# Kernel optimization log

Hardware: AMD Instinct MI355X
Metric: run time of the kernel (lower is better)

The kernel has to match this reference:

```python
import jax, jax.numpy as jnp
import numpy as np
import math

HID = 4096
SLOTS = 8
HEADS = 8
BD = 512  # bottleneck_dim
HD = BD // HEADS  # effective head dim = 64
B, S = 4, 4096


def setup_inputs() -> dict:
    key = jax.random.key(0)
    ks = jax.random.split(key, 8)
    std = 1.0 / math.sqrt(HID)
    return {
        "hidden_states": jax.random.normal(ks[0], (B, S, HID), dtype=jnp.float32),
        "attention_mask": jax.random.randint(ks[1], (B, S), 0, 2, dtype=jnp.int32),
        "memory_slots": jax.random.normal(ks[2], (SLOTS, HID), dtype=jnp.float32) * std,
        # torch nn.Linear weights are [out_features, in_features]
        "Wq": jax.random.normal(ks[3], (BD, HID), dtype=jnp.float32) * std,
        "Wk": jax.random.normal(ks[4], (BD, HID), dtype=jnp.float32) * std,
        "Wv": jax.random.normal(ks[5], (BD, HID), dtype=jnp.float32) * std,
        "Wo": jax.random.normal(ks[6], (HID, BD), dtype=jnp.float32) * (1.0 / math.sqrt(BD)),
    }


def reference(hidden_states, attention_mask, memory_slots, Wq, Wk, Wv, Wo):
    # Q from learnable slots (same for every batch element): [slots, BD]
    Q = memory_slots @ Wq.T
    Q = Q.reshape(SLOTS, HEADS, HD)                      # n h d
    # K/V from sequence: [b, s, BD] -> [b, s, h, d]
    K = jnp.einsum('bsi,oi->bso', hidden_states, Wk).reshape(B, S, HEADS, HD)
    V = jnp.einsum('bsi,oi->bso', hidden_states, Wv).reshape(B, S, HEADS, HD)
    # scores: [b, h, n, s]
    scores = jnp.einsum('nhd,bshd->bhns', Q, K) / jnp.sqrt(jnp.array(HD, scores_dtype := jnp.float32))
    mask = attention_mask[:, None, None, :]              # [b,1,1,s]
    scores = jnp.where(mask == 0, jnp.finfo(scores.dtype).min, scores)
    attn = jax.nn.softmax(scores, axis=-1)
    # output: [b, n, h, d] -> [b, n, BD]
    out = jnp.einsum('bhns,bshd->bnhd', attn, V).reshape(B, SLOTS, BD)
    # o_proj back to hidden_size
    return jnp.einsum('bnd,od->bno', out, Wo)            # [b, slots, HID]
```

## Files before the change

kernel.cpp:

```cpp
#include <hip/hip_runtime.h>
#include <math.h>

#define HID   4096
#define SLOTS 8
#define HEADS 8
#define BD    512
#define HD    64
#define BB    4
#define SS    4096
#define R64   64
#define LSTR  72

typedef __attribute__((ext_vector_type(8))) short bf16x8;
typedef __attribute__((ext_vector_type(4))) float f32x4;

__device__ __forceinline__ unsigned short f2bf(float x) {
  unsigned int u = __builtin_bit_cast(unsigned int, x);
  return (unsigned short)((u + 0x7fffu + ((u >> 16) & 1u)) >> 16);
}

__global__ void q_kernel(const float* __restrict__ ms, const float* __restrict__ Wq,
                         float* __restrict__ Q) {
  int w = (blockIdx.x * blockDim.x + threadIdx.x) >> 6;
  int lane = threadIdx.x & 63;
  if (w >= SLOTS * BD) return;
  int n = w >> 9, o = w & (BD - 1);
  const float* a = ms + n * HID;
  const float* b = Wq + (size_t)o * HID;
  float acc = 0.f;
  for (int i = lane; i < HID; i += 64) acc = fmaf(a[i], b[i], acc);
  #pragma unroll
  for (int off = 32; off; off >>= 1) acc += __shfl_down(acc, off, 64);
  if (lane == 0) Q[w] = acc;
}

__global__ void qw_kernel(const float* __restrict__ Q, const float* __restrict__ Wk,
                          unsigned short* __restrict__ QW) {
  int idx = blockIdx.x * blockDim.x + threadIdx.x;
  int r = idx >> 12, i = idx & (HID - 1);
  int h = r >> 3, n = r & 7;
  const float* q  = Q + n * BD + h * HD;
  const float* wk = Wk + (size_t)(h * HD) * HID + i;
  float acc = 0.f;
  #pragma unroll 8
  for (int d = 0; d < HD; ++d) acc = fmaf(q[d], wk[(size_t)d * HID], acc);
  QW[idx] = f2bf(acc * 0.125f);
}

__global__ __launch_bounds__(256) void scores_mfma(const float* __restrict__ hs,
                                                   const unsigned short* __restrict__ QW,
                                                   float* __restrict__ sp) {
  __shared__ unsigned short As[64 * LSTR];
  __shared__ unsigned short Bs[64 * LSTR];
  const int stile = blockIdx.x, b = blockIdx.y;
  const int tid = threadIdx.x;
  const int wv = tid >> 6, lane = tid & 63;
  const int quad = lane >> 4, l16 = lane & 15;
  const int srow = tid >> 2, kc = (tid & 3) << 4;
  const float* hsp = hs + ((size_t)(b * SS + stile * 64 + srow)) * HID + kc;
  const unsigned short* qwp = QW + (size_t)srow * HID + kc;

  f32x4 acc[4] = {};
  float4 fa0 = *(const float4*)(hsp + 0);
  float4 fa1 = *(const float4*)(hsp + 4);
  float4 fa2 = *(const float4*)(hsp + 8);
  float4 fa3 = *(const float4*)(hsp + 12);
  uint4 qb0 = *(const uint4*)(qwp);
  uint4 qb1 = *(const uint4*)(qwp + 8);

  for (int c = 0; c < 64; ++c) {
    __syncthreads();
    union { unsigned short us[16]; uint4 q[2]; } u;
    float f[16] = {fa0.x, fa0.y, fa0.z, fa0.w, fa1.x, fa1.y, fa1.z, fa1.w,
                   fa2.x, fa2.y, fa2.z, fa2.w, fa3.x, fa3.y, fa3.z, fa3.w};
    #pragma unroll
    for (int j = 0; j < 16; ++j) u.us[j] = f2bf(f[j]);
    *(uint4*)&As[srow * LSTR + kc]     = u.q[0];
    *(uint4*)&As[srow * LSTR + kc + 8] = u.q[1];
    *(uint4*)&Bs[srow * LSTR + kc]     = qb0;
    *(uint4*)&Bs[srow * LSTR + kc + 8] = qb1;
    __syncthreads();
    if (c < 63) {
      const float* p = hsp + (size_t)(c + 1) * 64;
      fa0 = *(const float4*)(p + 0);
      fa1 = *(const float4*)(p + 4);
      fa2 = *(const float4*)(p + 8);
      fa3 = *(const float4*)(p + 12);
      const unsigned short* q = qwp + (size_t)(c + 1) * 64;
      qb0 = *(const uint4*)(q);
      qb1 = *(const uint4*)(q + 8);
    }
    #pragma unroll
    for (int ks = 0; ks < 2; ++ks) {
      bf16x8 bfrag = *(const bf16x8*)&Bs[(wv * 16 + l16) * LSTR + ks * 32 + quad * 8];
      #pragma unroll
      for (int mt = 0; mt < 4; ++mt) {
        bf16x8 afrag = *(const bf16x8*)&As[(mt * 16 + l16) * LSTR + ks * 32 + quad * 8];
        acc[mt] = __builtin_amdgcn_mfma_f32_16x16x32_bf16(afrag, bfrag, acc[mt], 0, 0, 0);
      }
    }
  }
  const int r = wv * 16 + l16;
  #pragma unroll
  for (int mt = 0; mt < 4; ++mt) {
    int s = stile * 64 + mt * 16 + quad * 4;
    float4 v = make_float4(acc[mt][0], acc[mt][1], acc[mt][2], acc[mt][3]);
    *(float4*)(sp + ((size_t)(b * R64 + r)) * SS + s) = v;
  }
}

__global__ __launch_bounds__(256) void softmax_kernel(const float* __restrict__ sp,
                                                      const int* __restrict__ mask,
                                                      unsigned short* __restrict__ attn) {
  int br = blockIdx.x;
  int b = br >> 6;
  int tid = threadIdx.x;
  const float* row = sp + (size_t)br * SS;
  const int* mrow = mask + b * SS;
  float vals[16];
  float mx = -INFINITY;
  #pragma unroll
  for (int j = 0; j < 16; ++j) {
    int s = tid + j * 256;
    float v = row[s];
    if (mrow[s] == 0) v = -INFINITY;
    vals[j] = v;
    mx = fmaxf(mx, v);
  }
  __shared__ float redm[4], reds[4];
  #pragma unroll
  for (int off = 32; off; off >>= 1) mx = fmaxf(mx, __shfl_down(mx, off, 64));
  if ((tid & 63) == 0) redm[tid >> 6] = mx;
  __syncthreads();
  mx = fmaxf(fmaxf(redm[0], redm[1]), fmaxf(redm[2], redm[3]));
  float sum = 0.f;
  #pragma unroll
  for (int j = 0; j < 16; ++j) { vals[j] = expf(vals[j] - mx); sum += vals[j]; }
  #pragma unroll
  for (int off = 32; off; off >>= 1) sum += __shfl_down(sum, off, 64);
  if ((tid & 63) == 0) reds[tid >> 6] = sum;
  __syncthreads();
  sum = reds[0] + reds[1] + reds[2] + reds[3];
  float inv = 1.f / sum;
  #pragma unroll
  for (int j = 0; j < 16; ++j)
    attn[(size_t)br * SS + tid + j * 256] = f2bf(vals[j] * inv);
}

__global__ __launch_bounds__(256) void ctx_mfma(const unsigned short* __restrict__ attn,
                                                const float* __restrict__ hs,
                                                float* __restrict__ ctx) {
  __shared__ unsigned short As[64 * LSTR];
  __shared__ unsigned short Bs[64 * LSTR];
  const int itile = blockIdx.x, b = blockIdx.y;
  const int tid = threadIdx.x;
  const int wv = tid >> 6, lane = tid & 63;
  const int quad = lane >> 4, l16 = lane & 15;
  const int arow = tid >> 2, asc = (tid & 3) << 4;
  const unsigned short* ap = attn + ((size_t)(b * R64 + arow)) * SS + asc;
  const int p = tid & 31, g = tid >> 5;
  const float* bp0 = hs + ((size_t)(b * SS + 2 * p)) * HID + itile * 64 + g * 8;
  const float* bp1 = bp0 + HID;

  f32x4 acc[4] = {};
  uint4 aa0 = *(const uint4*)(ap);
  uint4 aa1 = *(const uint4*)(ap + 8);
  float4 hb00 = *(const float4*)(bp0);
  float4 hb01 = *(const float4*)(bp0 + 4);
  float4 hb10 = *(const float4*)(bp1);
  float4 hb11 = *(const float4*)(bp1 + 4);

  for (int c = 0; c < 64; ++c) {
    __syncthreads();
    *(uint4*)&As[arow * LSTR + asc]     = aa0;
    *(uint4*)&As[arow * LSTR + asc + 8] = aa1;
    {
      float lo[8] = {hb00.x, hb00.y, hb00.z, hb00.w, hb01.x, hb01.y, hb01.z, hb01.w};
      float hi[8] = {hb10.x, hb10.y, hb10.z, hb10.w, hb11.x, hb11.y, hb11.z, hb11.w};
      #pragma unroll
      for (int j = 0; j < 8; ++j) {
        unsigned int v = (unsigned int)f2bf(lo[j]) | ((unsigned int)f2bf(hi[j]) << 16);
        ((unsigned int*)Bs)[(g * 8 + j) * (LSTR / 2) + p] = v;
      }
    }
    __syncthreads();
    if (c < 63) {
      const unsigned short* an = ap + (size_t)(c + 1) * 64;
      aa0 = *(const uint4*)(an);
      aa1 = *(const uint4*)(an + 8);
      const float* bn0 = bp0 + (size_t)(c + 1) * 64 * HID;
      const float* bn1 = bn0 + HID;
      hb00 = *(const float4*)(bn0);
      hb01 = *(const float4*)(bn0 + 4);
      hb10 = *(const float4*)(bn1);
      hb11 = *(const float4*)(bn1 + 4);
    }
    #pragma unroll
    for (int ks = 0; ks < 2; ++ks) {
      bf16x8 bfrag = *(const bf16x8*)&Bs[(wv * 16 + l16) * LSTR + ks * 32 + quad * 8];
      #pragma unroll
      for (int mt = 0; mt < 4; ++mt) {
        bf16x8 afrag = *(const bf16x8*)&As[(mt * 16 + l16) * LSTR + ks * 32 + quad * 8];
        acc[mt] = __builtin_amdgcn_mfma_f32_16x16x32_bf16(afrag, bfrag, acc[mt], 0, 0, 0);
      }
    }
  }
  const int i = itile * 64 + wv * 16 + l16;
  #pragma unroll
  for (int mt = 0; mt < 4; ++mt) {
    int r0 = mt * 16 + quad * 4;
    #pragma unroll
    for (int j = 0; j < 4; ++j)
      ctx[((size_t)(b * R64 + r0 + j)) * HID + i] = acc[mt][j];
  }
}

__global__ void out_kernel(const float* __restrict__ ctx, const float* __restrict__ Wv,
                           float* __restrict__ out) {
  int w = (blockIdx.x * blockDim.x + threadIdx.x) >> 6;
  int lane = threadIdx.x & 63;
  if (w >= BB * SLOTS * BD) return;
  int b = w >> 12, n = (w >> 9) & 7, hd = w & 511, h = hd >> 6;
  const float* c  = ctx + ((size_t)b * R64 + h * 8 + n) * HID;
  const float* wv = Wv + (size_t)hd * HID;
  float acc = 0.f;
  for (int i = lane; i < HID; i += 64) acc = fmaf(c[i], wv[i], acc);
  #pragma unroll
  for (int off = 32; off; off >>= 1) acc += __shfl_down(acc, off, 64);
  if (lane == 0) out[w] = acc;
}

__global__ void final_kernel(const float* __restrict__ out, const float* __restrict__ Wo,
                             float* __restrict__ y) {
  int w = (blockIdx.x * blockDim.x + threadIdx.x) >> 6;
  int lane = threadIdx.x & 63;
  if (w >= BB * SLOTS * HID) return;
  int bn = w >> 12, o = w & 4095;
  const float* orow = out + bn * BD;
  const float* wo = Wo + (size_t)o * BD;
  float acc = 0.f;
  #pragma unroll
  for (int d = lane; d < BD; d += 64) acc = fmaf(orow[d], wo[d], acc);
  #pragma unroll
  for (int off = 32; off; off >>= 1) acc += __shfl_down(acc, off, 64);
  if (lane == 0) y[w] = acc;
}

extern "C" void kernel_launch(void* const* d_in, const int* in_sizes, int n_in,
                              void* d_out, int out_size, void* d_ws, size_t ws_size,
                              hipStream_t stream) {
  const float* hs   = (const float*)d_in[0];
  const int*   mask = (const int*)d_in[1];
  const float* ms   = (const float*)d_in[2];
  const float* Wq   = (const float*)d_in[3];
  const float* Wk   = (const float*)d_in[4];
  const float* Wv   = (const float*)d_in[5];
  const float* Wo   = (const float*)d_in[6];

  char* ws = (char*)d_ws;
  float*          Q    = (float*)ws;                    ws += 4096 * 4;
  unsigned short* QW   = (unsigned short*)ws;           ws += R64 * HID * 2;
  float*          sp   = (float*)ws;                    ws += (size_t)BB * R64 * SS * 4;
  unsigned short* attn = (unsigned short*)ws;           ws += (size_t)BB * R64 * SS * 2;
  float*          ctx  = (float*)ws;                    ws += (size_t)BB * R64 * HID * 4;
  float*          out  = (float*)ws;

  q_kernel<<<dim3((SLOTS * BD * 64) / 256), 256, 0, stream>>>(ms, Wq, Q);
  qw_kernel<<<dim3((R64 * HID) / 256), 256, 0, stream>>>(Q, Wk, QW);
  scores_mfma<<<dim3(64, 4), 256, 0, stream>>>(hs, QW, sp);
  softmax_kernel<<<dim3(BB * R64), 256, 0, stream>>>(sp, mask, attn);
  ctx_mfma<<<dim3(64, 4), 256, 0, stream>>>(attn, hs, ctx);
  out_kernel<<<dim3(4096), 256, 0, stream>>>(ctx, Wv, out);
  final_kernel<<<dim3(32768), 256, 0, stream>>>(out, Wo, (float*)d_out);
}
```

Baseline: 580.3 us.

## Split-K scores and ctx GEMMs, cache bf16 hidden states, swizzle LDS

Both the scores and context MFMA kernels now split their reduction dimension four ways (grid 64x4x4 instead of 64x4), which raises the block count from 256 to 1024 so the device is filled. The partial sums are added in softmax and out_kernel. The scores kernel also writes a bf16 copy of hidden_states, which the ctx kernel reads instead of the fp32 tensor. This halves the bytes of the second large pass and removes its conversion. LDS tiles switch from padded rows to an XOR swizzle. In exchange the kernels use extra workspace and write and read back 4x partial buffers.

```diff
diff --git a/kernel.cpp b/kernel.cpp
--- a/kernel.cpp
+++ b/kernel.cpp
@@ -9,7 +9,6 @@
 #define BB    4
 #define SS    4096
 #define R64   64
-#define LSTR  72
 
 typedef __attribute__((ext_vector_type(8))) short bf16x8;
 typedef __attribute__((ext_vector_type(4))) float f32x4;
@@ -18,6 +17,7 @@
   unsigned int u = __builtin_bit_cast(unsigned int, x);
   return (unsigned short)((u + 0x7fffu + ((u >> 16) & 1u)) >> 16);
 }
+
 
 __global__ void q_kernel(const float* __restrict__ ms, const float* __restrict__ Wq,
                          float* __restrict__ Q) {
@@ -47,18 +47,27 @@
   QW[idx] = f2bf(acc * 0.125f);
 }
 
-__global__ __launch_bounds__(256) void scores_mfma(const float* __restrict__ hs,
-                                                   const unsigned short* __restrict__ QW,
-                                                   float* __restrict__ sp) {
-  __shared__ unsigned short As[64 * LSTR];
-  __shared__ unsigned short Bs[64 * LSTR];
-  const int stile = blockIdx.x, b = blockIdx.y;
+__global__ __launch_bounds__(256, 4) void scores_mfma(const float* __restrict__ hs,
+                                                      const unsigned short* __restrict__ QW,
+                                                      float* __restrict__ sp,
+                                                      unsigned short* __restrict__ hsbf) {
+  __shared__ unsigned short As[64 * 64];
+  __shared__ unsigned short Bs[64 * 64];
+  const int stile = blockIdx.x, ks = blockIdx.y, b = blockIdx.z;
   const int tid = threadIdx.x;
   const int wv = tid >> 6, lane = tid & 63;
   const int quad = lane >> 4, l16 = lane & 15;
   const int srow = tid >> 2, kc = (tid & 3) << 4;
-  const float* hsp = hs + ((size_t)(b * SS + stile * 64 + srow)) * HID + kc;
-  const unsigned short* qwp = QW + (size_t)srow * HID + kc;
+  const int ch0 = (tid & 3) << 1;
+  const int sw = srow & 7;
+  const size_t arowoff = (size_t)(b * SS + stile * 64 + srow) * HID + ks * 1024 + kc;
+  const float* hsp = hs + arowoff;
+  unsigned short* hso = hsbf + arowoff;
+  const unsigned short* qwp = QW + (size_t)srow * HID + ks * 1024 + kc;
+  unsigned short* asw0 = &As[srow * 64 + (((ch0 + 0) ^ sw) << 3)];
+  unsigned short* asw1 = &As[srow * 64 + (((ch0 + 1) ^ sw) << 3)];
+  unsigned short* bsw0 = &Bs[srow * 64 + (((ch0 + 0) ^ sw) << 3)];
+  unsigned short* bsw1 = &Bs[srow * 64 + (((ch0 + 1) ^ sw) << 3)];
 
   f32x4 acc[4] = {};
   float4 fa0 = *(const float4*)(hsp + 0);
@@ -68,19 +77,21 @@
   uint4 qb0 = *(const uint4*)(qwp);
   uint4 qb1 = *(const uint4*)(qwp + 8);
 
-  for (int c = 0; c < 64; ++c) {
+  for (int c = 0; c < 16; ++c) {
     __syncthreads();
     union { unsigned short us[16]; uint4 q[2]; } u;
     float f[16] = {fa0.x, fa0.y, fa0.z, fa0.w, fa1.x, fa1.y, fa1.z, fa1.w,
                    fa2.x, fa2.y, fa2.z, fa2.w, fa3.x, fa3.y, fa3.z, fa3.w};
     #pragma unroll
     for (int j = 0; j < 16; ++j) u.us[j] = f2bf(f[j]);
-    *(uint4*)&As[srow * LSTR + kc]     = u.q[0];
-    *(uint4*)&As[srow * LSTR + kc + 8] = u.q[1];
-    *(uint4*)&Bs[srow * LSTR + kc]     = qb0;
-    *(uint4*)&Bs[srow * LSTR + kc + 8] = qb1;
-    __syncthreads();
-    if (c < 63) {
+    *(uint4*)asw0 = u.q[0];
+    *(uint4*)asw1 = u.q[1];
+    *(uint4*)bsw0 = qb0;
+    *(uint4*)bsw1 = qb1;
+    *(uint4*)(hso + (size_t)c * 64)     = u.q[0];
+    *(uint4*)(hso + (size_t)c * 64 + 8) = u.q[1];
+    __syncthreads();
+    if (c < 15) {
       const float* p = hsp + (size_t)(c + 1) * 64;
       fa0 = *(const float4*)(p + 0);
       fa1 = *(const float4*)(p + 4);
@@ -91,11 +102,13 @@
       qb1 = *(const uint4*)(q + 8);
     }
     #pragma unroll
-    for (int ks = 0; ks < 2; ++ks) {
-      bf16x8 bfrag = *(const bf16x8*)&Bs[(wv * 16 + l16) * LSTR + ks * 32 + quad * 8];
+    for (int kk = 0; kk < 2; ++kk) {
+      const int nrow = wv * 16 + l16;
+      bf16x8 bfrag = *(const bf16x8*)&Bs[nrow * 64 + (((kk * 4 + quad) ^ (nrow & 7)) << 3)];
       #pragma unroll
       for (int mt = 0; mt < 4; ++mt) {
-        bf16x8 afrag = *(const bf16x8*)&As[(mt * 16 + l16) * LSTR + ks * 32 + quad * 8];
+        const int mrow = mt * 16 + l16;
+        bf16x8 afrag = *(const bf16x8*)&As[mrow * 64 + (((kk * 4 + quad) ^ (mrow & 7)) << 3)];
         acc[mt] = __builtin_amdgcn_mfma_f32_16x16x32_bf16(afrag, bfrag, acc[mt], 0, 0, 0);
       }
     }
@@ -105,7 +118,7 @@
   for (int mt = 0; mt < 4; ++mt) {
     int s = stile * 64 + mt * 16 + quad * 4;
     float4 v = make_float4(acc[mt][0], acc[mt][1], acc[mt][2], acc[mt][3]);
-    *(float4*)(sp + ((size_t)(b * R64 + r)) * SS + s) = v;
+    *(float4*)(sp + (((size_t)ks * BB + b) * R64 + r) * SS + s) = v;
   }
 }
 
@@ -115,14 +128,15 @@
   int br = blockIdx.x;
   int b = br >> 6;
   int tid = threadIdx.x;
-  const float* row = sp + (size_t)br * SS;
   const int* mrow = mask + b * SS;
+  const size_t kstride = (size_t)BB * R64 * SS;
   float vals[16];
   float mx = -INFINITY;
   #pragma unroll
   for (int j = 0; j < 16; ++j) {
     int s = tid + j * 256;
-    float v = row[s];
+    size_t o = (size_t)br * SS + s;
+    float v = sp[o] + sp[o + kstride] + sp[o + 2 * kstride] + sp[o + 3 * kstride];
     if (mrow[s] == 0) v = -INFINITY;
     vals[j] = v;
     mx = fmaxf(mx, v);
@@ -147,60 +161,63 @@
     attn[(size_t)br * SS + tid + j * 256] = f2bf(vals[j] * inv);
 }
 
-__global__ __launch_bounds__(256) void ctx_mfma(const unsigned short* __restrict__ attn,
-                                                const float* __restrict__ hs,
-                                                float* __restrict__ ctx) {
-  __shared__ unsigned short As[64 * LSTR];
-  __shared__ unsigned short Bs[64 * LSTR];
-  const int itile = blockIdx.x, b = blockIdx.y;
+__global__ __launch_bounds__(256, 4) void ctx_mfma(const unsigned short* __restrict__ attn,
+                                                   const unsigned short* __restrict__ hsbf,
+                                                   float* __restrict__ cp) {
+  __shared__ unsigned short As[64 * 64];
+  __shared__ unsigned short Bs[64 * 64];
+  const int itile = blockIdx.x, ss = blockIdx.y, b = blockIdx.z;
   const int tid = threadIdx.x;
   const int wv = tid >> 6, lane = tid & 63;
   const int quad = lane >> 4, l16 = lane & 15;
   const int arow = tid >> 2, asc = (tid & 3) << 4;
-  const unsigned short* ap = attn + ((size_t)(b * R64 + arow)) * SS + asc;
+  const int ch0 = (tid & 3) << 1, swa = arow & 7;
+  const unsigned short* ap = attn + (size_t)(b * R64 + arow) * SS + ss * 1024 + asc;
+  unsigned short* asw0 = &As[arow * 64 + (((ch0 + 0) ^ swa) << 3)];
+  unsigned short* asw1 = &As[arow * 64 + (((ch0 + 1) ^ swa) << 3)];
   const int p = tid & 31, g = tid >> 5;
-  const float* bp0 = hs + ((size_t)(b * SS + 2 * p)) * HID + itile * 64 + g * 8;
-  const float* bp1 = bp0 + HID;
+  const unsigned short* bp0 = hsbf + (size_t)(b * SS + ss * 1024 + 2 * p) * HID + itile * 64 + g * 8;
+  const unsigned short* bp1 = bp0 + HID;
 
   f32x4 acc[4] = {};
   uint4 aa0 = *(const uint4*)(ap);
   uint4 aa1 = *(const uint4*)(ap + 8);
-  float4 hb00 = *(const float4*)(bp0);
-  float4 hb01 = *(const float4*)(bp0 + 4);
-  float4 hb10 = *(const float4*)(bp1);
-  float4 hb11 = *(const float4*)(bp1 + 4);
-
-  for (int c = 0; c < 64; ++c) {
-    __syncthreads();
-    *(uint4*)&As[arow * LSTR + asc]     = aa0;
-    *(uint4*)&As[arow * LSTR + asc + 8] = aa1;
+  uint4 hb0 = *(const uint4*)(bp0);
+  uint4 hb1 = *(const uint4*)(bp1);
+
+  for (int c = 0; c < 16; ++c) {
+    __syncthreads();
+    *(uint4*)asw0 = aa0;
+    *(uint4*)asw1 = aa1;
     {
-      float lo[8] = {hb00.x, hb00.y, hb00.z, hb00.w, hb01.x, hb01.y, hb01.z, hb01.w};
-      float hi[8] = {hb10.x, hb10.y, hb10.z, hb10.w, hb11.x, hb11.y, hb11.z, hb11.w};
+      unsigned int lo[4] = {hb0.x, hb0.y, hb0.z, hb0.w};
+      unsigned int hi[4] = {hb1.x, hb1.y, hb1.z, hb1.w};
       #pragma unroll
-      for (int j = 0; j < 8; ++j) {
-        unsigned int v = (unsigned int)f2bf(lo[j]) | ((unsigned int)f2bf(hi[j]) << 16);
-        ((unsigned int*)Bs)[(g * 8 + j) * (LSTR / 2) + p] = v;
+      for (int t = 0; t < 4; ++t) {
+        unsigned int d0 = (lo[t] & 0xffffu) | (hi[t] << 16);
+        unsigned int d1 = (lo[t] >> 16) | (hi[t] & 0xffff0000u);
+        int i0 = g * 8 + 2 * t, i1 = i0 + 1;
+        ((unsigned int*)Bs)[i0 * 32 + (((p >> 2) ^ (i0 & 7)) << 2) + (p & 3)] = d0;
+        ((unsigned int*)Bs)[i1 * 32 + (((p >> 2) ^ (i1 & 7)) << 2) + (p & 3)] = d1;
       }
     }
     __syncthreads();
-    if (c < 63) {
+    if (c < 15) {
       const unsigned short* an = ap + (size_t)(c + 1) * 64;
       aa0 = *(const uint4*)(an);
       aa1 = *(const uint4*)(an + 8);
-      const float* bn0 = bp0 + (size_t)(c + 1) * 64 * HID;
-      const float* bn1 = bn0 + HID;
-      hb00 = *(const float4*)(bn0);
-      hb01 = *(const float4*)(bn0 + 4);
-      hb10 = *(const float4*)(bn1);
-      hb11 = *(const float4*)(bn1 + 4);
-    }
-    #pragma unroll
-    for (int ks = 0; ks < 2; ++ks) {
-      bf16x8 bfrag = *(const bf16x8*)&Bs[(wv * 16 + l16) * LSTR + ks * 32 + quad * 8];
+      const unsigned short* bn0 = bp0 + (size_t)(c + 1) * 64 * HID;
+      hb0 = *(const uint4*)(bn0);
+      hb1 = *(const uint4*)(bn0 + HID);
+    }
+    #pragma unroll
+    for (int kk = 0; kk < 2; ++kk) {
+      const int nrow = wv * 16 + l16;
+      bf16x8 bfrag = *(const bf16x8*)&Bs[nrow * 64 + (((kk * 4 + quad) ^ (nrow & 7)) << 3)];
       #pragma unroll
       for (int mt = 0; mt < 4; ++mt) {
-        bf16x8 afrag = *(const bf16x8*)&As[(mt * 16 + l16) * LSTR + ks * 32 + quad * 8];
+        const int mrow = mt * 16 + l16;
+        bf16x8 afrag = *(const bf16x8*)&As[mrow * 64 + (((kk * 4 + quad) ^ (mrow & 7)) << 3)];
         acc[mt] = __builtin_amdgcn_mfma_f32_16x16x32_bf16(afrag, bfrag, acc[mt], 0, 0, 0);
       }
     }
@@ -211,20 +228,24 @@
     int r0 = mt * 16 + quad * 4;
     #pragma unroll
     for (int j = 0; j < 4; ++j)
-      ctx[((size_t)(b * R64 + r0 + j)) * HID + i] = acc[mt][j];
-  }
-}
-
-__global__ void out_kernel(const float* __restrict__ ctx, const float* __restrict__ Wv,
+      cp[(((size_t)ss * BB + b) * R64 + r0 + j) * HID + i] = acc[mt][j];
+  }
+}
+
+__global__ void out_kernel(const float* __restrict__ cp, const float* __restrict__ Wv,
                            float* __restrict__ out) {
   int w = (blockIdx.x * blockDim.x + threadIdx.x) >> 6;
   int lane = threadIdx.x & 63;
   if (w >= BB * SLOTS * BD) return;
   int b = w >> 12, n = (w >> 9) & 7, hd = w & 511, h = hd >> 6;
-  const float* c  = ctx + ((size_t)b * R64 + h * 8 + n) * HID;
+  const size_t sstride = (size_t)BB * R64 * HID;
+  const float* c  = cp + ((size_t)b * R64 + h * 8 + n) * HID;
   const float* wv = Wv + (size_t)hd * HID;
   float acc = 0.f;
-  for (int i = lane; i < HID; i += 64) acc = fmaf(c[i], wv[i], acc);
+  for (int i = lane; i < HID; i += 64) {
+    float s = c[i] + c[i + sstride] + c[i + 2 * sstride] + c[i + 3 * sstride];
+    acc = fmaf(s, wv[i], acc);
+  }
   #pragma unroll
   for (int off = 32; off; off >>= 1) acc += __shfl_down(acc, off, 64);
   if (lane == 0) out[w] = acc;
@@ -258,18 +279,19 @@
   const float* Wo   = (const float*)d_in[6];
 
   char* ws = (char*)d_ws;
-  float*          Q    = (float*)ws;                    ws += 4096 * 4;
-  unsigned short* QW   = (unsigned short*)ws;           ws += R64 * HID * 2;
-  float*          sp   = (float*)ws;                    ws += (size_t)BB * R64 * SS * 4;
-  unsigned short* attn = (unsigned short*)ws;           ws += (size_t)BB * R64 * SS * 2;
-  float*          ctx  = (float*)ws;                    ws += (size_t)BB * R64 * HID * 4;
+  float*          Q    = (float*)ws;          ws += 4096 * 4;
+  unsigned short* QW   = (unsigned short*)ws; ws += (size_t)R64 * HID * 2;
+  float*          sp   = (float*)ws;          ws += (size_t)4 * BB * R64 * SS * 4;
+  unsigned short* attn = (unsigned short*)ws; ws += (size_t)BB * R64 * SS * 2;
+  float*          cp   = (float*)ws;          ws += (size_t)4 * BB * R64 * HID * 4;
+  unsigned short* hsbf = (unsigned short*)ws; ws += (size_t)BB * SS * HID * 2;
   float*          out  = (float*)ws;
 
   q_kernel<<<dim3((SLOTS * BD * 64) / 256), 256, 0, stream>>>(ms, Wq, Q);
   qw_kernel<<<dim3((R64 * HID) / 256), 256, 0, stream>>>(Q, Wk, QW);
-  scores_mfma<<<dim3(64, 4), 256, 0, stream>>>(hs, QW, sp);
+  scores_mfma<<<dim3(64, 4, 4), 256, 0, stream>>>(hs, QW, sp, hsbf);
   softmax_kernel<<<dim3(BB * R64), 256, 0, stream>>>(sp, mask, attn);
-  ctx_mfma<<<dim3(64, 4), 256, 0, stream>>>(attn, hs, ctx);
-  out_kernel<<<dim3(4096), 256, 0, stream>>>(ctx, Wv, out);
+  ctx_mfma<<<dim3(64, 4, 4), 256, 0, stream>>>(attn, hsbf, cp);
+  out_kernel<<<dim3(4096), 256, 0, stream>>>(cp, Wv, out);
   final_kernel<<<dim3(32768), 256, 0, stream>>>(out, Wo, (float*)d_out);
 }
```

Result: no change. 582.8 us (+0.4%).

## Fuse softmax into scores GEMM and split ctx GEMM over sequence

Applied to the files above, without the earlier changes.

The scores kernel now loads operands straight from global memory into MFMA registers with no LDS staging. It also applies the mask and exponentiates in place, writing unnormalized bf16 attention plus per-tile partial denominators, so the fp32 score buffer and the separate softmax pass go away. The ctx GEMM is split four ways along the sequence to get more blocks in flight, and a reduce kernel sums the partials and applies the inverse denominator. Dropping the max subtraction relies on scores staying small enough that exp cannot overflow. The change also adds two small kernels and a partial-sum buffer.

```diff
diff --git a/kernel.cpp b/kernel.cpp
--- a/kernel.cpp
+++ b/kernel.cpp
@@ -9,7 +9,6 @@
 #define BB    4
 #define SS    4096
 #define R64   64
-#define LSTR  72
 
 typedef __attribute__((ext_vector_type(8))) short bf16x8;
 typedef __attribute__((ext_vector_type(4))) float f32x4;
@@ -17,6 +16,10 @@
 __device__ __forceinline__ unsigned short f2bf(float x) {
   unsigned int u = __builtin_bit_cast(unsigned int, x);
   return (unsigned short)((u + 0x7fffu + ((u >> 16) & 1u)) >> 16);
+}
+__device__ __forceinline__ float bf2f(unsigned short h) {
+  unsigned int u = ((unsigned int)h) << 16;
+  return __builtin_bit_cast(float, u);
 }
 
 __global__ void q_kernel(const float* __restrict__ ms, const float* __restrict__ Wq,
@@ -49,170 +52,154 @@
 
 __global__ __launch_bounds__(256) void scores_mfma(const float* __restrict__ hs,
                                                    const unsigned short* __restrict__ QW,
-                                                   float* __restrict__ sp) {
-  __shared__ unsigned short As[64 * LSTR];
-  __shared__ unsigned short Bs[64 * LSTR];
+                                                   const int* __restrict__ mask,
+                                                   unsigned short* __restrict__ attn,
+                                                   float* __restrict__ denomp) {
+  __shared__ float denw[256];
   const int stile = blockIdx.x, b = blockIdx.y;
   const int tid = threadIdx.x;
   const int wv = tid >> 6, lane = tid & 63;
   const int quad = lane >> 4, l16 = lane & 15;
-  const int srow = tid >> 2, kc = (tid & 3) << 4;
-  const float* hsp = hs + ((size_t)(b * SS + stile * 64 + srow)) * HID + kc;
-  const unsigned short* qwp = QW + (size_t)srow * HID + kc;
+  const int s = stile * 64 + wv * 16 + l16;
+  const float* bp = hs + ((size_t)b * SS + s) * HID + quad * 8;
+  const unsigned short* ap = QW + (size_t)l16 * HID + quad * 8;
 
   f32x4 acc[4] = {};
-  float4 fa0 = *(const float4*)(hsp + 0);
-  float4 fa1 = *(const float4*)(hsp + 4);
-  float4 fa2 = *(const float4*)(hsp + 8);
-  float4 fa3 = *(const float4*)(hsp + 12);
-  uint4 qb0 = *(const uint4*)(qwp);
-  uint4 qb1 = *(const uint4*)(qwp + 8);
-
-  for (int c = 0; c < 64; ++c) {
-    __syncthreads();
-    union { unsigned short us[16]; uint4 q[2]; } u;
-    float f[16] = {fa0.x, fa0.y, fa0.z, fa0.w, fa1.x, fa1.y, fa1.z, fa1.w,
-                   fa2.x, fa2.y, fa2.z, fa2.w, fa3.x, fa3.y, fa3.z, fa3.w};
-    #pragma unroll
-    for (int j = 0; j < 16; ++j) u.us[j] = f2bf(f[j]);
-    *(uint4*)&As[srow * LSTR + kc]     = u.q[0];
-    *(uint4*)&As[srow * LSTR + kc + 8] = u.q[1];
-    *(uint4*)&Bs[srow * LSTR + kc]     = qb0;
-    *(uint4*)&Bs[srow * LSTR + kc + 8] = qb1;
-    __syncthreads();
-    if (c < 63) {
-      const float* p = hsp + (size_t)(c + 1) * 64;
-      fa0 = *(const float4*)(p + 0);
-      fa1 = *(const float4*)(p + 4);
-      fa2 = *(const float4*)(p + 8);
-      fa3 = *(const float4*)(p + 12);
-      const unsigned short* q = qwp + (size_t)(c + 1) * 64;
-      qb0 = *(const uint4*)(q);
-      qb1 = *(const uint4*)(q + 8);
+  float4 cb0 = *(const float4*)(bp),      cb1 = *(const float4*)(bp + 4);
+  uint4  ca0 = *(const uint4*)(ap);
+  uint4  ca1 = *(const uint4*)(ap + 16 * HID);
+  uint4  ca2 = *(const uint4*)(ap + 32 * HID);
+  uint4  ca3 = *(const uint4*)(ap + 48 * HID);
+  float4 nb0 = *(const float4*)(bp + 32), nb1 = *(const float4*)(bp + 36);
+  uint4  na0 = *(const uint4*)(ap + 32);
+  uint4  na1 = *(const uint4*)(ap + 16 * HID + 32);
+  uint4  na2 = *(const uint4*)(ap + 32 * HID + 32);
+  uint4  na3 = *(const uint4*)(ap + 48 * HID + 32);
+
+  for (int k0 = 0; k0 < 4096; k0 += 32) {
+    float4 fb0, fb1; uint4 fa0, fa1, fa2, fa3;
+    if (k0 + 64 < 4096) {
+      fb0 = *(const float4*)(bp + k0 + 64);
+      fb1 = *(const float4*)(bp + k0 + 68);
+      fa0 = *(const uint4*)(ap + k0 + 64);
+      fa1 = *(const uint4*)(ap + 16 * HID + k0 + 64);
+      fa2 = *(const uint4*)(ap + 32 * HID + k0 + 64);
+      fa3 = *(const uint4*)(ap + 48 * HID + k0 + 64);
+    } else {
+      fb0 = nb0; fb1 = nb1; fa0 = na0; fa1 = na1; fa2 = na2; fa3 = na3;
     }
-    #pragma unroll
-    for (int ks = 0; ks < 2; ++ks) {
-      bf16x8 bfrag = *(const bf16x8*)&Bs[(wv * 16 + l16) * LSTR + ks * 32 + quad * 8];
-      #pragma unroll
-      for (int mt = 0; mt < 4; ++mt) {
-        bf16x8 afrag = *(const bf16x8*)&As[(mt * 16 + l16) * LSTR + ks * 32 + quad * 8];
-        acc[mt] = __builtin_amdgcn_mfma_f32_16x16x32_bf16(afrag, bfrag, acc[mt], 0, 0, 0);
-      }
+    float f[8] = {cb0.x, cb0.y, cb0.z, cb0.w, cb1.x, cb1.y, cb1.z, cb1.w};
+    union { unsigned short us[8]; bf16x8 v; } ub;
+    #pragma unroll
+    for (int j = 0; j < 8; ++j) ub.us[j] = f2bf(f[j]);
+    acc[0] = __builtin_amdgcn_mfma_f32_16x16x32_bf16(__builtin_bit_cast(bf16x8, ca0), ub.v, acc[0], 0, 0, 0);
+    acc[1] = __builtin_amdgcn_mfma_f32_16x16x32_bf16(__builtin_bit_cast(bf16x8, ca1), ub.v, acc[1], 0, 0, 0);
+    acc[2] = __builtin_amdgcn_mfma_f32_16x16x32_bf16(__builtin_bit_cast(bf16x8, ca2), ub.v, acc[2], 0, 0, 0);
+    acc[3] = __builtin_amdgcn_mfma_f32_16x16x32_bf16(__builtin_bit_cast(bf16x8, ca3), ub.v, acc[3], 0, 0, 0);
+    cb0 = nb0; cb1 = nb1; ca0 = na0; ca1 = na1; ca2 = na2; ca3 = na3;
+    nb0 = fb0; nb1 = fb1; na0 = fa0; na1 = fa1; na2 = fa2; na3 = fa3;
+  }
+
+  const int mk = mask[b * SS + s];
+  float er[16];
+  #pragma unroll
+  for (int mt = 0; mt < 4; ++mt)
+    #pragma unroll
+    for (int j = 0; j < 4; ++j) {
+      float e = mk ? __expf(acc[mt][j]) : 0.f;
+      unsigned short h = f2bf(e);
+      attn[((size_t)b * R64 + mt * 16 + quad * 4 + j) * SS + s] = h;
+      er[mt * 4 + j] = bf2f(h);
     }
-  }
-  const int r = wv * 16 + l16;
-  #pragma unroll
-  for (int mt = 0; mt < 4; ++mt) {
-    int s = stile * 64 + mt * 16 + quad * 4;
-    float4 v = make_float4(acc[mt][0], acc[mt][1], acc[mt][2], acc[mt][3]);
-    *(float4*)(sp + ((size_t)(b * R64 + r)) * SS + s) = v;
-  }
-}
-
-__global__ __launch_bounds__(256) void softmax_kernel(const float* __restrict__ sp,
-                                                      const int* __restrict__ mask,
-                                                      unsigned short* __restrict__ attn) {
-  int br = blockIdx.x;
-  int b = br >> 6;
-  int tid = threadIdx.x;
-  const float* row = sp + (size_t)br * SS;
-  const int* mrow = mask + b * SS;
-  float vals[16];
-  float mx = -INFINITY;
-  #pragma unroll
-  for (int j = 0; j < 16; ++j) {
-    int s = tid + j * 256;
-    float v = row[s];
-    if (mrow[s] == 0) v = -INFINITY;
-    vals[j] = v;
-    mx = fmaxf(mx, v);
-  }
-  __shared__ float redm[4], reds[4];
-  #pragma unroll
-  for (int off = 32; off; off >>= 1) mx = fmaxf(mx, __shfl_down(mx, off, 64));
-  if ((tid & 63) == 0) redm[tid >> 6] = mx;
+  #pragma unroll
+  for (int v = 0; v < 16; ++v) {
+    float e = er[v];
+    #pragma unroll
+    for (int xm = 1; xm < 16; xm <<= 1) e += __shfl_xor(e, xm, 64);
+    er[v] = e;
+  }
+  if (l16 == 0) {
+    #pragma unroll
+    for (int mt = 0; mt < 4; ++mt)
+      #pragma unroll
+      for (int j = 0; j < 4; ++j)
+        denw[wv * 64 + mt * 16 + quad * 4 + j] = er[mt * 4 + j];
+  }
   __syncthreads();
-  mx = fmaxf(fmaxf(redm[0], redm[1]), fmaxf(redm[2], redm[3]));
-  float sum = 0.f;
-  #pragma unroll
-  for (int j = 0; j < 16; ++j) { vals[j] = expf(vals[j] - mx); sum += vals[j]; }
-  #pragma unroll
-  for (int off = 32; off; off >>= 1) sum += __shfl_down(sum, off, 64);
-  if ((tid & 63) == 0) reds[tid >> 6] = sum;
-  __syncthreads();
-  sum = reds[0] + reds[1] + reds[2] + reds[3];
-  float inv = 1.f / sum;
-  #pragma unroll
-  for (int j = 0; j < 16; ++j)
-    attn[(size_t)br * SS + tid + j * 256] = f2bf(vals[j] * inv);
+  if (tid < 64)
+    denomp[((size_t)b * R64 + tid) * 64 + stile] =
+        denw[tid] + denw[64 + tid] + denw[128 + tid] + denw[192 + tid];
+}
+
+__global__ void invden_kernel(const float* __restrict__ denomp, float* __restrict__ invden) {
+  int t = threadIdx.x;
+  const float4* p = (const float4*)(denomp + (size_t)t * 64);
+  float s = 0.f;
+  #pragma unroll
+  for (int j = 0; j < 16; ++j) { float4 v = p[j]; s += v.x + v.y + v.z + v.w; }
+  invden[t] = 1.f / s;
 }
 
 __global__ __launch_bounds__(256) void ctx_mfma(const unsigned short* __restrict__ attn,
                                                 const float* __restrict__ hs,
-                                                float* __restrict__ ctx) {
-  __shared__ unsigned short As[64 * LSTR];
-  __shared__ unsigned short Bs[64 * LSTR];
-  const int itile = blockIdx.x, b = blockIdx.y;
+                                                float* __restrict__ cp) {
+  const int itile = blockIdx.x, ssb = blockIdx.y, b = blockIdx.z;
   const int tid = threadIdx.x;
   const int wv = tid >> 6, lane = tid & 63;
   const int quad = lane >> 4, l16 = lane & 15;
-  const int arow = tid >> 2, asc = (tid & 3) << 4;
-  const unsigned short* ap = attn + ((size_t)(b * R64 + arow)) * SS + asc;
-  const int p = tid & 31, g = tid >> 5;
-  const float* bp0 = hs + ((size_t)(b * SS + 2 * p)) * HID + itile * 64 + g * 8;
-  const float* bp1 = bp0 + HID;
+  const int i = itile * 64 + wv * 16 + l16;
+  const unsigned short* ap = attn + ((size_t)b * R64 + l16) * SS + ssb * 1024 + quad * 8;
+  const float* bp = hs + ((size_t)(b * SS) + ssb * 1024 + quad * 8) * HID + i;
 
   f32x4 acc[4] = {};
-  uint4 aa0 = *(const uint4*)(ap);
-  uint4 aa1 = *(const uint4*)(ap + 8);
-  float4 hb00 = *(const float4*)(bp0);
-  float4 hb01 = *(const float4*)(bp0 + 4);
-  float4 hb10 = *(const float4*)(bp1);
-  float4 hb11 = *(const float4*)(bp1 + 4);
-
-  for (int c = 0; c < 64; ++c) {
-    __syncthreads();
-    *(uint4*)&As[arow * LSTR + asc]     = aa0;
-    *(uint4*)&As[arow * LSTR + asc + 8] = aa1;
-    {
-      float lo[8] = {hb00.x, hb00.y, hb00.z, hb00.w, hb01.x, hb01.y, hb01.z, hb01.w};
-      float hi[8] = {hb10.x, hb10.y, hb10.z, hb10.w, hb11.x, hb11.y, hb11.z, hb11.w};
-      #pragma unroll
-      for (int j = 0; j < 8; ++j) {
-        unsigned int v = (unsigned int)f2bf(lo[j]) | ((unsigned int)f2bf(hi[j]) << 16);
-        ((unsigned int*)Bs)[(g * 8 + j) * (LSTR / 2) + p] = v;
-      }
+  uint4 ca[4], na[4];
+  float cb[8], nb[8];
+  #pragma unroll
+  for (int mt = 0; mt < 4; ++mt) ca[mt] = *(const uint4*)(ap + mt * 16 * SS);
+  #pragma unroll
+  for (int j = 0; j < 8; ++j) cb[j] = bp[j * HID];
+  #pragma unroll
+  for (int mt = 0; mt < 4; ++mt) na[mt] = *(const uint4*)(ap + mt * 16 * SS + 32);
+  #pragma unroll
+  for (int j = 0; j < 8; ++j) nb[j] = bp[(32 + j) * HID];
+
+  for (int s0 = 0; s0 < 1024; s0 += 32) {
+    uint4 fa[4]; float fb[8];
+    if (s0 + 64 < 1024) {
+      #pragma unroll
+      for (int mt = 0; mt < 4; ++mt) fa[mt] = *(const uint4*)(ap + mt * 16 * SS + s0 + 64);
+      #pragma unroll
+      for (int j = 0; j < 8; ++j) fb[j] = bp[(s0 + 64 + j) * HID];
+    } else {
+      #pragma unroll
+      for (int mt = 0; mt < 4; ++mt) fa[mt] = na[mt];
+      #pragma unroll
+      for (int j = 0; j < 8; ++j) fb[j] = nb[j];
     }
-    __syncthreads();
-    if (c < 63) {
-      const unsigned short* an = ap + (size_t)(c + 1) * 64;
-      aa0 = *(const uint4*)(an);
-      aa1 = *(const uint4*)(an + 8);
-      const float* bn0 = bp0 + (size_t)(c + 1) * 64 * HID;
-      const float* bn1 = bn0 + HID;
-      hb00 = *(const float4*)(bn0);
-      hb01 = *(const float4*)(bn0 + 4);
-      hb10 = *(const float4*)(bn1);
-      hb11 = *(const float4*)(bn1 + 4);
-    }
-    #pragma unroll
-    for (int ks = 0; ks < 2; ++ks) {
-      bf16x8 bfrag = *(const bf16x8*)&Bs[(wv * 16 + l16) * LSTR + ks * 32 + quad * 8];
-      #pragma unroll
-      for (int mt = 0; mt < 4; ++mt) {
-        bf16x8 afrag = *(const bf16x8*)&As[(mt * 16 + l16) * LSTR + ks * 32 + quad * 8];
-        acc[mt] = __builtin_amdgcn_mfma_f32_16x16x32_bf16(afrag, bfrag, acc[mt], 0, 0, 0);
-      }
-    }
-  }
-  const int i = itile * 64 + wv * 16 + l16;
-  #pragma unroll
-  for (int mt = 0; mt < 4; ++mt) {
-    int r0 = mt * 16 + quad * 4;
+    union { unsigned short us[8]; bf16x8 v; } ub;
+    #pragma unroll
+    for (int j = 0; j < 8; ++j) ub.us[j] = f2bf(cb[j]);
+    #pragma unroll
+    for (int mt = 0; mt < 4; ++mt)
+      acc[mt] = __builtin_amdgcn_mfma_f32_16x16x32_bf16(__builtin_bit_cast(bf16x8, ca[mt]), ub.v, acc[mt], 0, 0, 0);
+    #pragma unroll
+    for (int mt = 0; mt < 4; ++mt) { ca[mt] = na[mt]; na[mt] = fa[mt]; }
+    #pragma unroll
+    for (int j = 0; j < 8; ++j) { cb[j] = nb[j]; nb[j] = fb[j]; }
+  }
+  #pragma unroll
+  for (int mt = 0; mt < 4; ++mt)
     #pragma unroll
     for (int j = 0; j < 4; ++j)
-      ctx[((size_t)(b * R64 + r0 + j)) * HID + i] = acc[mt][j];
-  }
+      cp[(((size_t)ssb * BB + b) * R64 + mt * 16 + quad * 4 + j) * HID + i] = acc[mt][j];
+}
+
+__global__ void ctx_reduce(const float* __restrict__ cp, const float* __restrict__ invden,
+                           float* __restrict__ ctx) {
+  int idx = blockIdx.x * 256 + threadIdx.x;
+  const size_t n = (size_t)BB * R64 * HID;
+  float v = cp[idx] + cp[idx + n] + cp[idx + 2 * n] + cp[idx + 3 * n];
+  ctx[idx] = v * invden[idx >> 12];
 }
 
 __global__ void out_kernel(const float* __restrict__ ctx, const float* __restrict__ Wv,
@@ -258,18 +245,21 @@
   const float* Wo   = (const float*)d_in[6];
 
   char* ws = (char*)d_ws;
-  float*          Q    = (float*)ws;                    ws += 4096 * 4;
-  unsigned short* QW   = (unsigned short*)ws;           ws += R64 * HID * 2;
-  float*          sp   = (float*)ws;                    ws += (size_t)BB * R64 * SS * 4;
-  unsigned short* attn = (unsigned short*)ws;           ws += (size_t)BB * R64 * SS * 2;
-  float*          ctx  = (float*)ws;                    ws += (size_t)BB * R64 * HID * 4;
-  float*          out  = (float*)ws;
-
-  q_kernel<<<dim3((SLOTS * BD * 64) / 256), 256, 0, stream>>>(ms, Wq, Q);
+  float*          Q      = (float*)ws;          ws += 4096 * 4;
+  unsigned short* QW     = (unsigned short*)ws; ws += (size_t)R64 * HID * 2;
+  unsigned short* attn   = (unsigned short*)ws; ws += (size_t)BB * R64 * SS * 2;
+  float*          denomp = (float*)ws;          ws += 256 * 64 * 4;
+  float*          invden = (float*)ws;          ws += 256 * 4 + 3072;
+  float*          cp     = (float*)ws;          ws += (size_t)4 * BB * R64 * HID * 4;
+  float*          ctx    = (float*)ws;          ws += (size_t)BB * R64 * HID * 4;
+  float*          out    = (float*)ws;
+
+  q_kernel<<<dim3(1024), 256, 0, stream>>>(ms, Wq, Q);
   qw_kernel<<<dim3((R64 * HID) / 256), 256, 0, stream>>>(Q, Wk, QW);
-  scores_mfma<<<dim3(64, 4), 256, 0, stream>>>(hs, QW, sp);
-  softmax_kernel<<<dim3(BB * R64), 256, 0, stream>>>(sp, mask, attn);
-  ctx_mfma<<<dim3(64, 4), 256, 0, stream>>>(attn, hs, ctx);
+  scores_mfma<<<dim3(64, 4), 256, 0, stream>>>(hs, QW, mask, attn, denomp);
+  invden_kernel<<<dim3(1), 256, 0, stream>>>(denomp, invden);
+  ctx_mfma<<<dim3(64, 4, 4), 256, 0, stream>>>(attn, hs, cp);
+  ctx_reduce<<<dim3(4096), 256, 0, stream>>>(cp, invden, ctx);
   out_kernel<<<dim3(4096), 256, 0, stream>>>(ctx, Wv, out);
   final_kernel<<<dim3(32768), 256, 0, stream>>>(out, Wo, (float*)d_out);
 }
```

Result: slower. 620.1 us (+6.9%).
